# Performance work log

Measured on AMD Instinct MI355X. Metric: run time of the kernel, lower is better.

The kernel has to match this reference:

```python
import jax, jax.numpy as jnp
import numpy as np

PF = 8
BITS = 4
T, D, O, A = 1024, 2048, 4096, 4  # tokens, in_dim, per-slice out_dim, max_deltas


def _dequant(qw, qz, sc):
    """GPTQ-style 4-bit dequant, single quant group (g_idx all zero).
    qw: [O, D//PF] int32 (nibbles packed along input dim)
    qz: [O//PF, 1] int32 (zero nibbles packed along output dim)
    sc: [O, 1] float scales
    returns W: [O, D] float32
    """
    Od, Kp = qw.shape
    shifts = jnp.arange(PF, dtype=jnp.int32) * BITS
    q = ((qw[:, :, None] >> shifts) & 0xF).reshape(Od, Kp * PF).astype(jnp.float32)
    z = ((qz[:, 0][:, None] >> shifts) & 0xF).reshape(Od)[:, None].astype(jnp.float32)
    return sc.astype(jnp.float32) * (q - z)


def _delta_slice(x, indices, qw_s, qz_s, sc_s):
    # per-token adapter dispatch: tokens with indices==a use delta weight a
    out = jnp.zeros((x.shape[0], qw_s.shape[1]), dtype=jnp.float32)
    for a in range(qw_s.shape[0]):  # fixed small loop over adapters
        W = _dequant(qw_s[a], qz_s[a], sc_s[a])           # [O, D]
        xm = jnp.where((indices == a)[:, None], x, 0.0)    # gather-by-mask
        out = out + xm @ W.T                               # [T, O]
    return out


def setup_inputs() -> dict:
    key = jax.random.key(0)
    ks = jax.random.split(key, 10)
    MAXI = np.int32(2147483647)
    return {
        "x": jax.random.normal(ks[0], (T, D), dtype=jnp.float32),
        "base_weight": jax.random.normal(ks[1], (2 * O, D), dtype=jnp.float32) * 0.02,
        "base_bias": jax.random.normal(ks[2], (2 * O,), dtype=jnp.float32) * 0.02,
        "qweight_0": jax.random.randint(ks[3], (A, O, D // PF), 0, MAXI, dtype=jnp.int32),
        "qweight_1": jax.random.randint(ks[4], (A, O, D // PF), 0, MAXI, dtype=jnp.int32),
        "qzeros_0": jax.random.randint(ks[5], (A, O // PF, 1), 0, MAXI, dtype=jnp.int32),
        "qzeros_1": jax.random.randint(ks[6], (A, O // PF, 1), 0, MAXI, dtype=jnp.int32),
        "scales_0": jax.random.uniform(ks[7], (A, O, 1), dtype=jnp.float32) * 1e-3,
        "scales_1": jax.random.uniform(ks[8], (A, O, 1), dtype=jnp.float32) * 1e-3,
        "g_idx_0": jnp.zeros((D,), dtype=jnp.int32),
        "g_idx_1": jnp.zeros((D,), dtype=jnp.int32),
        "indices": jax.random.randint(ks[9], (T,), 0, A, dtype=jnp.int32),
    }


def reference(x, base_weight, base_bias, qweight_0, qweight_1, qzeros_0, qzeros_1,
              scales_0, scales_1, g_idx_0, g_idx_1, indices):
    # base ColumnParallelLinear GEMM (+bias, skip_bias_add=False)
    out = x @ base_weight.T + base_bias  # [T, 2*O]
    # apply_delta_packed_nslice onto the two equal output slices
    d0 = _delta_slice(x, indices, qweight_0, qzeros_0, scales_0)
    d1 = _delta_slice(x, indices, qweight_1, qzeros_1, scales_1)
    return out + jnp.concatenate([d0, d1], axis=1)
```

## Files before the change

kernel.cpp:

```cpp
#include <hip/hip_runtime.h>
#include <hip/hip_bf16.h>
#include <stdint.h>

#define T_TOK 1024
#define DIN   2048
#define NOUT  8192
#define OSL   4096
#define ROWS_PAD 1408
#define BM 128
#define BN 128
#define BK 32

typedef _Float16 f16x8 __attribute__((ext_vector_type(8)));
typedef _Float16 f16x2 __attribute__((ext_vector_type(2)));
typedef float    f32x4 __attribute__((ext_vector_type(4)));

__device__ __forceinline__ void gload16(const void* gp, void* lp) {
  __builtin_amdgcn_global_load_lds(
      (__attribute__((address_space(1))) void*)gp,
      (__attribute__((address_space(3))) void*)lp, 16, 0, 0);
}

__device__ __forceinline__ f16x2 u2h(uint32_t u) {
  union { uint32_t u; f16x2 h; } c; c.u = u; return c.h;
}

__device__ __forceinline__ f16x8 cvt_interleave(float4 f0, float4 f1) {
  f16x8 h;
  h[0] = (_Float16)f0.x; h[1] = (_Float16)f1.x;
  h[2] = (_Float16)f0.y; h[3] = (_Float16)f1.y;
  h[4] = (_Float16)f0.z; h[5] = (_Float16)f1.z;
  h[6] = (_Float16)f0.w; h[7] = (_Float16)f1.w;
  return h;
}

template<bool FULL>
__global__ void prep_all(const float* __restrict__ x, const float* __restrict__ wb,
                         const int* __restrict__ qw0, const int* __restrict__ qw1,
                         const int* __restrict__ qz0, const int* __restrict__ qz1,
                         const float* __restrict__ sc0, const float* __restrict__ sc1,
                         const int* __restrict__ indices,
                         _Float16* __restrict__ xh,
                         _Float16* __restrict__ wout,
                         int* __restrict__ inv, int* __restrict__ meta)
{
  const int b = blockIdx.x;
  const int tid = threadIdx.x;

  if (b == 0) {
    __shared__ int cnt[4], cur[4];
    if (tid < 4) cnt[tid] = 0;
    __syncthreads();
    for (int t = tid; t < T_TOK; t += 256) atomicAdd(&cnt[indices[t]], 1);
    __syncthreads();
    if (tid == 0) {
      int off = 0;
      for (int a = 0; a < 4; ++a) {
        meta[a] = off;
        meta[5 + a] = off + cnt[a];
        cur[a] = off;
        off = (off + cnt[a] + 127) & ~127;
      }
      meta[4] = off;
    }
    __syncthreads();
    for (int i = tid; i < ROWS_PAD; i += 256) inv[i] = -1;
    __syncthreads();
    for (int t = tid; t < T_TOK; t += 256) {
      int a = indices[t];
      int p = atomicAdd(&cur[a], 1);
      inv[p] = t;
    }
    return;
  }

  if (b <= 1 + T_TOK) {
    const int row = b - 1;
    const int d0 = tid * 8;
    f16x8 h;
    if (row < T_TOK) {
      const float* src = x + (size_t)row * DIN + d0;
      h = cvt_interleave(*(const float4*)src, *(const float4*)(src + 4));
    } else {
#pragma unroll
      for (int j = 0; j < 8; ++j) h[j] = (_Float16)0.0f;
    }
    *(f16x8*)(xh + (size_t)row * DIN + d0) = h;
    return;
  }

  const int n = b - (2 + T_TOK);
  const int d0 = tid * 8;
  const float* src = wb + (size_t)n * DIN + d0;
  union { f16x8 v; f16x2 p[4]; } wbr;
  wbr.v = cvt_interleave(*(const float4*)src, *(const float4*)(src + 4));

  if (!FULL) {
    *(f16x8*)(wout + (size_t)n * DIN + d0) = wbr.v;
    return;
  }

  const int sl = n >> 12;
  const int n_sl = n & (OSL - 1);
  const int* qw = sl ? qw1 : qw0;
  const int* qz = sl ? qz1 : qz0;
  const float* sc = sl ? sc1 : sc0;

#pragma unroll
  for (int a = 0; a < 4; ++a) {
    const uint32_t wv = (uint32_t)qw[((size_t)(a * OSL + n_sl)) * (DIN / 8) + tid];
    const int zw = qz[a * (OSL / 8) + (n_sl >> 3)];
    const float s = sc[(size_t)a * OSL + n_sl];
    const int z = (zw >> ((n_sl & 7) << 2)) & 0xF;
    f16x2 s2; s2[0] = s2[1] = (_Float16)s;
    f16x2 k2; k2[0] = k2[1] = (_Float16)(float)(-(1024 + z));
    union { f16x8 v; f16x2 p[4]; } h;
#pragma unroll
    for (int j = 0; j < 4; ++j) {
      uint32_t t0 = ((wv >> (4 * j)) & 0x000F000Fu) | 0x64006400u;
      h.p[j] = (u2h(t0) + k2) * s2 + wbr.p[j];
    }
    *(f16x8*)(wout + ((size_t)(a * NOUT) + n) * DIN + d0) = h.v;
  }
}

__global__ __launch_bounds__(256) void kslim(
    const _Float16* __restrict__ xh, const _Float16* __restrict__ weff,
    const float* __restrict__ bias,
    const int* __restrict__ inv, const int* __restrict__ meta,
    float* __restrict__ out)
{
  const int m0 = blockIdx.y * BM;
  if (m0 >= meta[4]) return;
  int ad = 0;
  if (m0 >= meta[1]) ad = 1;
  if (m0 >= meta[2]) ad = 2;
  if (m0 >= meta[3]) ad = 3;
  if (m0 >= meta[5 + ad]) return;

  const int n0 = blockIdx.x * BN;
  const int tid  = threadIdx.x;
  const int wave = tid >> 6;
  const int lane = tid & 63;
  const int quad = lane >> 4;
  const int l16  = lane & 15;
  const int wm = (wave & 1) << 6;
  const int wn = (wave >> 1) << 6;

  __shared__ __align__(16) char smem[16384];

  f32x4 acc[4][4];
#pragma unroll
  for (int i = 0; i < 4; ++i)
#pragma unroll
    for (int j = 0; j < 4; ++j) acc[i][j] = (f32x4)0.0f;

  const int kch = (((tid & 3) ^ ((tid >> 3) & 3)) << 3);
  const int rloc = tid >> 2;
  int r0 = inv[m0 + rloc];       if (r0 < 0) r0 = T_TOK;
  int r1 = inv[m0 + rloc + 64];  if (r1 < 0) r1 = T_TOK;
  const _Float16* ag0 = xh + (size_t)r0 * DIN + kch;
  const _Float16* ag1 = xh + (size_t)r1 * DIN + kch;
  const _Float16* bg0 = weff + ((size_t)(ad * NOUT) + n0 + rloc) * DIN + kch;
  const _Float16* bg1 = bg0 + (size_t)64 * DIN;
  char* sa0 = smem +         wave * 1024;
  char* sa1 = smem +  4096 + wave * 1024;
  char* sb0 = smem +  8192 + wave * 1024;
  char* sb1 = smem + 12288 + wave * 1024;

  const int qoff = ((quad ^ ((l16 >> 1) & 3)) << 4);

  for (int k0 = 0; k0 < DIN; k0 += BK) {
    gload16(ag0, sa0);
    gload16(ag1, sa1);
    gload16(bg0, sb0);
    gload16(bg1, sb1);
    __syncthreads();

    f16x8 af[4], bfr[4];
#pragma unroll
    for (int t = 0; t < 4; ++t)
      af[t] = *(const f16x8*)(smem + (wm + t * 16 + l16) * 64 + qoff);
#pragma unroll
    for (int t = 0; t < 4; ++t)
      bfr[t] = *(const f16x8*)(smem + 8192 + (wn + t * 16 + l16) * 64 + qoff);
#pragma unroll
    for (int mt = 0; mt < 4; ++mt)
#pragma unroll
      for (int nt = 0; nt < 4; ++nt)
        acc[mt][nt] = __builtin_amdgcn_mfma_f32_16x16x32_f16(af[mt], bfr[nt], acc[mt][nt], 0, 0, 0);
    __syncthreads();

    ag0 += BK; ag1 += BK; bg0 += BK; bg1 += BK;
  }

#pragma unroll
  for (int mt = 0; mt < 4; ++mt) {
    const int rowb = m0 + wm + mt * 16 + quad * 4;
    int tk[4];
#pragma unroll
    for (int r = 0; r < 4; ++r) tk[r] = inv[rowb + r];
#pragma unroll
    for (int nt = 0; nt < 4; ++nt) {
      const int col = n0 + wn + nt * 16 + l16;
      const float bv = bias[col];
#pragma unroll
      for (int r = 0; r < 4; ++r) {
        if (tk[r] >= 0)
          out[(size_t)tk[r] * NOUT + col] = acc[mt][nt][r] + bv;
      }
    }
  }
}

__global__ __launch_bounds__(256) void kdq(
    const _Float16* __restrict__ xh, const _Float16* __restrict__ wbh,
    const int* __restrict__ qw0, const int* __restrict__ qw1,
    const int* __restrict__ qz0, const int* __restrict__ qz1,
    const float* __restrict__ sc0, const float* __restrict__ sc1,
    const float* __restrict__ bias,
    const int* __restrict__ inv, const int* __restrict__ meta,
    float* __restrict__ out)
{
  const int m0 = blockIdx.y * BM;
  if (m0 >= meta[4]) return;
  int ad = 0;
  if (m0 >= meta[1]) ad = 1;
  if (m0 >= meta[2]) ad = 2;
  if (m0 >= meta[3]) ad = 3;
  if (m0 >= meta[5 + ad]) return;

  const int n0 = blockIdx.x * BN;
  const int sl = n0 >> 12;
  const int tid  = threadIdx.x;
  const int wave = tid >> 6;
  const int lane = tid & 63;
  const int quad = lane >> 4;
  const int l16  = lane & 15;
  const int wm = (wave & 1) << 6;
  const int wn = (wave >> 1) << 6;

  __shared__ __align__(16) char smem[16384];

  f32x4 acc[4][4];
#pragma unroll
  for (int i = 0; i < 4; ++i)
#pragma unroll
    for (int j = 0; j < 4; ++j) acc[i][j] = (f32x4)0.0f;

  const int kch = (((tid & 3) ^ ((tid >> 3) & 3)) << 3);
  const int rloc = tid >> 2;
  int r0 = inv[m0 + rloc];       if (r0 < 0) r0 = T_TOK;
  int r1 = inv[m0 + rloc + 64];  if (r1 < 0) r1 = T_TOK;
  const _Float16* ag0 = xh + (size_t)r0 * DIN + kch;
  const _Float16* ag1 = xh + (size_t)r1 * DIN + kch;
  char* sa0 = smem + wave * 1024;
  char* sa1 = smem + 4096 + wave * 1024;

  const int o_local = tid >> 1;
  const int o = n0 + o_local;
  const int o_sl = o & (OSL - 1);
  const int* qw = (sl ? qw1 : qw0) + ((size_t)ad * OSL + o_sl) * (DIN / 8) + ((tid & 1) << 1);
  const int zw = (sl ? qz1 : qz0)[ad * (OSL / 8) + (o_sl >> 3)];
  const float s = (sl ? sc1 : sc0)[(size_t)ad * OSL + o_sl];
  const int z = (zw >> ((o_sl & 7) << 2)) & 0xF;
  f16x2 s2; s2[0] = s2[1] = (_Float16)s;
  f16x2 k2; k2[0] = k2[1] = (_Float16)(float)(-(1024 + z));
  const _Float16* wbhp = wbh + (size_t)o * DIN + ((tid & 1) << 4);

  const int bswz = (o_local >> 1) & 3;
  char* bb = smem + 8192 + o_local * 64;
  char* bw0 = bb + (((((tid & 1) << 1)    ) ^ bswz) << 4);
  char* bw1 = bb + (((((tid & 1) << 1) | 1) ^ bswz) << 4);
  const int qoff = ((quad ^ ((l16 >> 1) & 3)) << 4);

  for (int k0 = 0; k0 < DIN; k0 += BK) {
    gload16(ag0, sa0);
    gload16(ag1, sa1);
    int2 wv = *(const int2*)qw;
    union { f16x8 v; f16x2 p[4]; } wA, wB;
    wA.v = *(const f16x8*)wbhp;
    wB.v = *(const f16x8*)(wbhp + 8);
    const uint32_t wx = (uint32_t)wv.x, wy = (uint32_t)wv.y;
    union { f16x8 v; f16x2 p[4]; } h0, h1;
#pragma unroll
    for (int j = 0; j < 4; ++j) {
      uint32_t t0 = ((wx >> (4 * j)) & 0x000F000Fu) | 0x64006400u;
      uint32_t t1 = ((wy >> (4 * j)) & 0x000F000Fu) | 0x64006400u;
      h0.p[j] = (u2h(t0) + k2) * s2 + wA.p[j];
      h1.p[j] = (u2h(t1) + k2) * s2 + wB.p[j];
    }
    *(f16x8*)bw0 = h0.v;
    *(f16x8*)bw1 = h1.v;
    __syncthreads();

    f16x8 af[4], bfr[4];
#pragma unroll
    for (int t = 0; t < 4; ++t)
      af[t] = *(const f16x8*)(smem + (wm + t * 16 + l16) * 64 + qoff);
#pragma unroll
    for (int t = 0; t < 4; ++t)
      bfr[t] = *(const f16x8*)(smem + 8192 + (wn + t * 16 + l16) * 64 + qoff);
#pragma unroll
    for (int mt = 0; mt < 4; ++mt)
#pragma unroll
      for (int nt = 0; nt < 4; ++nt)
        acc[mt][nt] = __builtin_amdgcn_mfma_f32_16x16x32_f16(af[mt], bfr[nt], acc[mt][nt], 0, 0, 0);
    __syncthreads();

    ag0 += BK; ag1 += BK; qw += 4; wbhp += BK;
  }

#pragma unroll
  for (int mt = 0; mt < 4; ++mt) {
    const int rowb = m0 + wm + mt * 16 + quad * 4;
    int tk[4];
#pragma unroll
    for (int r = 0; r < 4; ++r) tk[r] = inv[rowb + r];
#pragma unroll
    for (int nt = 0; nt < 4; ++nt) {
      const int col = n0 + wn + nt * 16 + l16;
      const float bv = bias[col];
#pragma unroll
      for (int r = 0; r < 4; ++r) {
        if (tk[r] >= 0)
          out[(size_t)tk[r] * NOUT + col] = acc[mt][nt][r] + bv;
      }
    }
  }
}

extern "C" void kernel_launch(void* const* d_in, const int* in_sizes, int n_in,
                              void* d_out, int out_size, void* d_ws, size_t ws_size,
                              hipStream_t stream) {
  const float* x    = (const float*)d_in[0];
  const float* wb   = (const float*)d_in[1];
  const float* bias = (const float*)d_in[2];
  const int*   qw0  = (const int*)d_in[3];
  const int*   qw1  = (const int*)d_in[4];
  const int*   qz0  = (const int*)d_in[5];
  const int*   qz1  = (const int*)d_in[6];
  const float* sc0  = (const float*)d_in[7];
  const float* sc1  = (const float*)d_in[8];
  const int*   indices = (const int*)d_in[11];
  float* out = (float*)d_out;

  char* w = (char*)d_ws;
  _Float16* xh = (_Float16*)w;
  size_t off = (size_t)(T_TOK + 1) * DIN * 2;
  int* inv  = (int*)(w + off);
  int* meta = inv + ROWS_PAD;
  size_t woff = (off + (size_t)ROWS_PAD * 4 + 64 + 255) & ~(size_t)255;
  _Float16* wout = (_Float16*)(w + woff);
  const bool full = ws_size >= woff + (size_t)4 * NOUT * DIN * 2;

  const int nprep = 2 + T_TOK + NOUT;
  dim3 g(NOUT / BN, ROWS_PAD / BM, 1);

  if (full) {
    prep_all<true><<<nprep, 256, 0, stream>>>(x, wb, qw0, qw1, qz0, qz1, sc0, sc1,
                                              indices, xh, wout, inv, meta);
    kslim<<<g, 256, 0, stream>>>(xh, wout, bias, inv, meta, out);
  } else {
    prep_all<false><<<nprep, 256, 0, stream>>>(x, wb, qw0, qw1, qz0, qz1, sc0, sc1,
                                               indices, xh, wout, inv, meta);
    kdq<<<g, 256, 0, stream>>>(xh, wout, qw0, qw1, qz0, qz1, sc0, sc1,
                               bias, inv, meta, out);
  }
}
```

Before: 227.7 us.

## Drop pre-dequantized weight path and software-pipeline fused dequant GEMM with double buffering

Removes the full-workspace path that materialized four dequantized fp16 effective weight matrices in the prep kernel. The fused dequant GEMM is now always used. It gets a double-buffered LDS pipeline with register prefetch of packed nibbles and base weights, explicit vmcnt/lgkmcnt waits, raw barriers and raised priority around the MFMAs. Block ids are remapped so neighbouring blocks share weight columns for better cache locality. This avoids writing and re-reading a large fp16 weight buffer, at the cost of redoing the dequant in every row tile and of more fragile hand scheduling.

```diff
diff --git a/kernel.cpp b/kernel.cpp
--- a/kernel.cpp
+++ b/kernel.cpp
@@ -1,5 +1,4 @@
 #include <hip/hip_runtime.h>
-#include <hip/hip_bf16.h>
 #include <stdint.h>
 
 #define T_TOK 1024
@@ -10,6 +9,8 @@
 #define BM 128
 #define BN 128
 #define BK 32
+#define NT (DIN / BK)
+#define BUF1 16384
 
 typedef _Float16 f16x8 __attribute__((ext_vector_type(8)));
 typedef _Float16 f16x2 __attribute__((ext_vector_type(2)));
@@ -34,15 +35,14 @@
   return h;
 }
 
-template<bool FULL>
-__global__ void prep_all(const float* __restrict__ x, const float* __restrict__ wb,
-                         const int* __restrict__ qw0, const int* __restrict__ qw1,
-                         const int* __restrict__ qz0, const int* __restrict__ qz1,
-                         const float* __restrict__ sc0, const float* __restrict__ sc1,
-                         const int* __restrict__ indices,
-                         _Float16* __restrict__ xh,
-                         _Float16* __restrict__ wout,
-                         int* __restrict__ inv, int* __restrict__ meta)
+#define VMCNT5() asm volatile("s_waitcnt vmcnt(5)" ::: "memory")
+#define VMCNT0() asm volatile("s_waitcnt vmcnt(0)" ::: "memory")
+#define LGKM0()  asm volatile("s_waitcnt lgkmcnt(0)" ::: "memory")
+
+__global__ void prep(const float* __restrict__ x, const float* __restrict__ wb,
+                     const int* __restrict__ indices,
+                     _Float16* __restrict__ xh, _Float16* __restrict__ wbh,
+                     int* __restrict__ inv, int* __restrict__ meta)
 {
   const int b = blockIdx.x;
   const int tid = threadIdx.x;
@@ -92,128 +92,11 @@
   const int n = b - (2 + T_TOK);
   const int d0 = tid * 8;
   const float* src = wb + (size_t)n * DIN + d0;
-  union { f16x8 v; f16x2 p[4]; } wbr;
-  wbr.v = cvt_interleave(*(const float4*)src, *(const float4*)(src + 4));
-
-  if (!FULL) {
-    *(f16x8*)(wout + (size_t)n * DIN + d0) = wbr.v;
-    return;
-  }
-
-  const int sl = n >> 12;
-  const int n_sl = n & (OSL - 1);
-  const int* qw = sl ? qw1 : qw0;
-  const int* qz = sl ? qz1 : qz0;
-  const float* sc = sl ? sc1 : sc0;
-
-#pragma unroll
-  for (int a = 0; a < 4; ++a) {
-    const uint32_t wv = (uint32_t)qw[((size_t)(a * OSL + n_sl)) * (DIN / 8) + tid];
-    const int zw = qz[a * (OSL / 8) + (n_sl >> 3)];
-    const float s = sc[(size_t)a * OSL + n_sl];
-    const int z = (zw >> ((n_sl & 7) << 2)) & 0xF;
-    f16x2 s2; s2[0] = s2[1] = (_Float16)s;
-    f16x2 k2; k2[0] = k2[1] = (_Float16)(float)(-(1024 + z));
-    union { f16x8 v; f16x2 p[4]; } h;
-#pragma unroll
-    for (int j = 0; j < 4; ++j) {
-      uint32_t t0 = ((wv >> (4 * j)) & 0x000F000Fu) | 0x64006400u;
-      h.p[j] = (u2h(t0) + k2) * s2 + wbr.p[j];
-    }
-    *(f16x8*)(wout + ((size_t)(a * NOUT) + n) * DIN + d0) = h.v;
-  }
-}
-
-__global__ __launch_bounds__(256) void kslim(
-    const _Float16* __restrict__ xh, const _Float16* __restrict__ weff,
-    const float* __restrict__ bias,
-    const int* __restrict__ inv, const int* __restrict__ meta,
-    float* __restrict__ out)
-{
-  const int m0 = blockIdx.y * BM;
-  if (m0 >= meta[4]) return;
-  int ad = 0;
-  if (m0 >= meta[1]) ad = 1;
-  if (m0 >= meta[2]) ad = 2;
-  if (m0 >= meta[3]) ad = 3;
-  if (m0 >= meta[5 + ad]) return;
-
-  const int n0 = blockIdx.x * BN;
-  const int tid  = threadIdx.x;
-  const int wave = tid >> 6;
-  const int lane = tid & 63;
-  const int quad = lane >> 4;
-  const int l16  = lane & 15;
-  const int wm = (wave & 1) << 6;
-  const int wn = (wave >> 1) << 6;
-
-  __shared__ __align__(16) char smem[16384];
-
-  f32x4 acc[4][4];
-#pragma unroll
-  for (int i = 0; i < 4; ++i)
-#pragma unroll
-    for (int j = 0; j < 4; ++j) acc[i][j] = (f32x4)0.0f;
-
-  const int kch = (((tid & 3) ^ ((tid >> 3) & 3)) << 3);
-  const int rloc = tid >> 2;
-  int r0 = inv[m0 + rloc];       if (r0 < 0) r0 = T_TOK;
-  int r1 = inv[m0 + rloc + 64];  if (r1 < 0) r1 = T_TOK;
-  const _Float16* ag0 = xh + (size_t)r0 * DIN + kch;
-  const _Float16* ag1 = xh + (size_t)r1 * DIN + kch;
-  const _Float16* bg0 = weff + ((size_t)(ad * NOUT) + n0 + rloc) * DIN + kch;
-  const _Float16* bg1 = bg0 + (size_t)64 * DIN;
-  char* sa0 = smem +         wave * 1024;
-  char* sa1 = smem +  4096 + wave * 1024;
-  char* sb0 = smem +  8192 + wave * 1024;
-  char* sb1 = smem + 12288 + wave * 1024;
-
-  const int qoff = ((quad ^ ((l16 >> 1) & 3)) << 4);
-
-  for (int k0 = 0; k0 < DIN; k0 += BK) {
-    gload16(ag0, sa0);
-    gload16(ag1, sa1);
-    gload16(bg0, sb0);
-    gload16(bg1, sb1);
-    __syncthreads();
-
-    f16x8 af[4], bfr[4];
-#pragma unroll
-    for (int t = 0; t < 4; ++t)
-      af[t] = *(const f16x8*)(smem + (wm + t * 16 + l16) * 64 + qoff);
-#pragma unroll
-    for (int t = 0; t < 4; ++t)
-      bfr[t] = *(const f16x8*)(smem + 8192 + (wn + t * 16 + l16) * 64 + qoff);
-#pragma unroll
-    for (int mt = 0; mt < 4; ++mt)
-#pragma unroll
-      for (int nt = 0; nt < 4; ++nt)
-        acc[mt][nt] = __builtin_amdgcn_mfma_f32_16x16x32_f16(af[mt], bfr[nt], acc[mt][nt], 0, 0, 0);
-    __syncthreads();
-
-    ag0 += BK; ag1 += BK; bg0 += BK; bg1 += BK;
-  }
-
-#pragma unroll
-  for (int mt = 0; mt < 4; ++mt) {
-    const int rowb = m0 + wm + mt * 16 + quad * 4;
-    int tk[4];
-#pragma unroll
-    for (int r = 0; r < 4; ++r) tk[r] = inv[rowb + r];
-#pragma unroll
-    for (int nt = 0; nt < 4; ++nt) {
-      const int col = n0 + wn + nt * 16 + l16;
-      const float bv = bias[col];
-#pragma unroll
-      for (int r = 0; r < 4; ++r) {
-        if (tk[r] >= 0)
-          out[(size_t)tk[r] * NOUT + col] = acc[mt][nt][r] + bv;
-      }
-    }
-  }
-}
-
-__global__ __launch_bounds__(256) void kdq(
+  f16x8 v = cvt_interleave(*(const float4*)src, *(const float4*)(src + 4));
+  *(f16x8*)(wbh + (size_t)n * DIN + d0) = v;
+}
+
+__global__ __launch_bounds__(256) void kfuse(
     const _Float16* __restrict__ xh, const _Float16* __restrict__ wbh,
     const int* __restrict__ qw0, const int* __restrict__ qw1,
     const int* __restrict__ qz0, const int* __restrict__ qz1,
@@ -222,7 +105,10 @@
     const int* __restrict__ inv, const int* __restrict__ meta,
     float* __restrict__ out)
 {
-  const int m0 = blockIdx.y * BM;
+  const int id = blockIdx.y * 64 + blockIdx.x;
+  const int m0 = (id >> 6) * BM;
+  const int n0 = (((id & 7) << 3) | ((id >> 3) & 7)) * BN;
+
   if (m0 >= meta[4]) return;
   int ad = 0;
   if (m0 >= meta[1]) ad = 1;
@@ -230,7 +116,6 @@
   if (m0 >= meta[3]) ad = 3;
   if (m0 >= meta[5 + ad]) return;
 
-  const int n0 = blockIdx.x * BN;
   const int sl = n0 >> 12;
   const int tid  = threadIdx.x;
   const int wave = tid >> 6;
@@ -240,7 +125,7 @@
   const int wm = (wave & 1) << 6;
   const int wn = (wave >> 1) << 6;
 
-  __shared__ __align__(16) char smem[16384];
+  __shared__ __align__(16) char smem[32768];
 
   f32x4 acc[4][4];
 #pragma unroll
@@ -254,62 +139,109 @@
   int r1 = inv[m0 + rloc + 64];  if (r1 < 0) r1 = T_TOK;
   const _Float16* ag0 = xh + (size_t)r0 * DIN + kch;
   const _Float16* ag1 = xh + (size_t)r1 * DIN + kch;
-  char* sa0 = smem + wave * 1024;
-  char* sa1 = smem + 4096 + wave * 1024;
+  const int saoff0 = wave * 1024;
+  const int saoff1 = 4096 + wave * 1024;
 
   const int o_local = tid >> 1;
   const int o = n0 + o_local;
   const int o_sl = o & (OSL - 1);
-  const int* qw = (sl ? qw1 : qw0) + ((size_t)ad * OSL + o_sl) * (DIN / 8) + ((tid & 1) << 1);
+  const int* qwp = (sl ? qw1 : qw0) + ((size_t)ad * OSL + o_sl) * (DIN / 8) + ((tid & 1) << 1);
   const int zw = (sl ? qz1 : qz0)[ad * (OSL / 8) + (o_sl >> 3)];
   const float s = (sl ? sc1 : sc0)[(size_t)ad * OSL + o_sl];
   const int z = (zw >> ((o_sl & 7) << 2)) & 0xF;
   f16x2 s2; s2[0] = s2[1] = (_Float16)s;
   f16x2 k2; k2[0] = k2[1] = (_Float16)(float)(-(1024 + z));
-  const _Float16* wbhp = wbh + (size_t)o * DIN + ((tid & 1) << 4);
+  const _Float16* wbp = wbh + (size_t)o * DIN + ((tid & 1) << 4);
 
   const int bswz = (o_local >> 1) & 3;
-  char* bb = smem + 8192 + o_local * 64;
-  char* bw0 = bb + (((((tid & 1) << 1)    ) ^ bswz) << 4);
-  char* bw1 = bb + (((((tid & 1) << 1) | 1) ^ bswz) << 4);
+  const int bwoff0 = 8192 + o_local * 64 + (((((tid & 1) << 1)    ) ^ bswz) << 4);
+  const int bwoff1 = 8192 + o_local * 64 + (((((tid & 1) << 1) | 1) ^ bswz) << 4);
   const int qoff = ((quad ^ ((l16 >> 1) & 3)) << 4);
 
-  for (int k0 = 0; k0 < DIN; k0 += BK) {
-    gload16(ag0, sa0);
-    gload16(ag1, sa1);
-    int2 wv = *(const int2*)qw;
-    union { f16x8 v; f16x2 p[4]; } wA, wB;
-    wA.v = *(const f16x8*)wbhp;
-    wB.v = *(const f16x8*)(wbhp + 8);
-    const uint32_t wx = (uint32_t)wv.x, wy = (uint32_t)wv.y;
-    union { f16x8 v; f16x2 p[4]; } h0, h1;
+  auto LOADREGS = [&](int t, int2 &qv, f16x8 &wa, f16x8 &wb2) {
+    qv  = *(const int2*)(qwp + t * 4);
+    wa  = *(const f16x8*)(wbp + t * BK);
+    wb2 = *(const f16x8*)(wbp + t * BK + 8);
+  };
+  auto GLOADS = [&](int bb, int t) {
+    gload16(ag0 + t * BK, smem + bb + saoff0);
+    gload16(ag1 + t * BK, smem + bb + saoff1);
+  };
+  auto DEQW = [&](int bb, int2 qv, f16x8 wa, f16x8 wb2) {
+    const uint32_t wx = (uint32_t)qv.x, wy = (uint32_t)qv.y;
+    union U { f16x8 v; f16x2 p[4]; } A_, B_, h0, h1;
+    A_.v = wa; B_.v = wb2;
 #pragma unroll
     for (int j = 0; j < 4; ++j) {
       uint32_t t0 = ((wx >> (4 * j)) & 0x000F000Fu) | 0x64006400u;
       uint32_t t1 = ((wy >> (4 * j)) & 0x000F000Fu) | 0x64006400u;
-      h0.p[j] = (u2h(t0) + k2) * s2 + wA.p[j];
-      h1.p[j] = (u2h(t1) + k2) * s2 + wB.p[j];
-    }
-    *(f16x8*)bw0 = h0.v;
-    *(f16x8*)bw1 = h1.v;
-    __syncthreads();
-
-    f16x8 af[4], bfr[4];
+      h0.p[j] = (u2h(t0) + k2) * s2 + A_.p[j];
+      h1.p[j] = (u2h(t1) + k2) * s2 + B_.p[j];
+    }
+    *(f16x8*)(smem + bb + bwoff0) = h0.v;
+    *(f16x8*)(smem + bb + bwoff1) = h1.v;
+  };
+  auto COMPUTE = [&](int bb) {
+    f16x8 af[4], bf[4];
 #pragma unroll
     for (int t = 0; t < 4; ++t)
-      af[t] = *(const f16x8*)(smem + (wm + t * 16 + l16) * 64 + qoff);
+      af[t] = *(const f16x8*)(smem + bb + (wm + t * 16 + l16) * 64 + qoff);
 #pragma unroll
     for (int t = 0; t < 4; ++t)
-      bfr[t] = *(const f16x8*)(smem + 8192 + (wn + t * 16 + l16) * 64 + qoff);
+      bf[t] = *(const f16x8*)(smem + bb + 8192 + (wn + t * 16 + l16) * 64 + qoff);
+    __builtin_amdgcn_s_setprio(1);
 #pragma unroll
     for (int mt = 0; mt < 4; ++mt)
 #pragma unroll
       for (int nt = 0; nt < 4; ++nt)
-        acc[mt][nt] = __builtin_amdgcn_mfma_f32_16x16x32_f16(af[mt], bfr[nt], acc[mt][nt], 0, 0, 0);
-    __syncthreads();
-
-    ag0 += BK; ag1 += BK; qw += 4; wbhp += BK;
-  }
+        acc[mt][nt] = __builtin_amdgcn_mfma_f32_16x16x32_f16(af[mt], bf[nt], acc[mt][nt], 0, 0, 0);
+    __builtin_amdgcn_s_setprio(0);
+  };
+
+  int2 qvA, qvB;
+  f16x8 waA, wbA2, waB, wbB2;
+
+  LOADREGS(0, qvA, waA, wbA2);
+  GLOADS(0, 0);
+  LOADREGS(1, qvB, waB, wbB2);
+  GLOADS(BUF1, 1);
+  VMCNT5();
+  __builtin_amdgcn_sched_barrier(0);
+  DEQW(0, qvA, waA, wbA2);
+  LGKM0();
+  __builtin_amdgcn_s_barrier();
+
+  for (int t = 0; t < NT - 2; t += 2) {
+    LOADREGS(t + 2, qvA, waA, wbA2);
+    COMPUTE(0);
+    __builtin_amdgcn_s_barrier();
+    __builtin_amdgcn_sched_barrier(0);
+    GLOADS(0, t + 2);
+    VMCNT5();
+    __builtin_amdgcn_sched_barrier(0);
+    DEQW(BUF1, qvB, waB, wbB2);
+    LGKM0();
+    __builtin_amdgcn_s_barrier();
+
+    LOADREGS(t + 3, qvB, waB, wbB2);
+    COMPUTE(BUF1);
+    __builtin_amdgcn_s_barrier();
+    __builtin_amdgcn_sched_barrier(0);
+    GLOADS(BUF1, t + 3);
+    VMCNT5();
+    __builtin_amdgcn_sched_barrier(0);
+    DEQW(0, qvA, waA, wbA2);
+    LGKM0();
+    __builtin_amdgcn_s_barrier();
+  }
+
+  COMPUTE(0);
+  VMCNT0();
+  __builtin_amdgcn_sched_barrier(0);
+  DEQW(BUF1, qvB, waB, wbB2);
+  LGKM0();
+  __builtin_amdgcn_s_barrier();
+  COMPUTE(BUF1);
 
 #pragma unroll
   for (int mt = 0; mt < 4; ++mt) {
@@ -351,20 +283,9 @@
   int* inv  = (int*)(w + off);
   int* meta = inv + ROWS_PAD;
   size_t woff = (off + (size_t)ROWS_PAD * 4 + 64 + 255) & ~(size_t)255;
-  _Float16* wout = (_Float16*)(w + woff);
-  const bool full = ws_size >= woff + (size_t)4 * NOUT * DIN * 2;
-
-  const int nprep = 2 + T_TOK + NOUT;
-  dim3 g(NOUT / BN, ROWS_PAD / BM, 1);
-
-  if (full) {
-    prep_all<true><<<nprep, 256, 0, stream>>>(x, wb, qw0, qw1, qz0, qz1, sc0, sc1,
-                                              indices, xh, wout, inv, meta);
-    kslim<<<g, 256, 0, stream>>>(xh, wout, bias, inv, meta, out);
-  } else {
-    prep_all<false><<<nprep, 256, 0, stream>>>(x, wb, qw0, qw1, qz0, qz1, sc0, sc1,
-                                               indices, xh, wout, inv, meta);
-    kdq<<<g, 256, 0, stream>>>(xh, wout, qw0, qw1, qz0, qz1, sc0, sc1,
-                               bias, inv, meta, out);
-  }
-}
+  _Float16* wbh = (_Float16*)(w + woff);
+
+  prep<<<2 + T_TOK + NOUT, 256, 0, stream>>>(x, wb, indices, xh, wbh, inv, meta);
+  kfuse<<<dim3(64, 11), 256, 0, stream>>>(xh, wbh, qw0, qw1, qz0, qz1, sc0, sc1,
+                                          bias, inv, meta, out);
+}
```

New measurement: 247.0 us. 1.08x slower.

## Double-buffer LDS tiles in grouped GEMM kernel to overlap loads with MFMA

Applied to the files above, without the earlier changes.

The first GEMM kernel now uses two LDS buffers (32 KB instead of 16 KB). It issues the global-to-LDS loads for tile k+1 while running MFMAs on tile k, and drops one barrier per iteration. The goal is to hide global memory latency that the single-buffer load, sync, compute, sync loop left exposed. Doubling LDS use may lower occupancy. The second kernel only swaps BK for a literal 32 and is otherwise unchanged.

```diff
diff --git a/kernel.cpp b/kernel.cpp
--- a/kernel.cpp
+++ b/kernel.cpp
@@ -10,6 +10,8 @@
 #define BM 128
 #define BN 128
 #define BK 32
+#define NT (DIN / BK)
+#define BUFS 16384
 
 typedef _Float16 f16x8 __attribute__((ext_vector_type(8)));
 typedef _Float16 f16x2 __attribute__((ext_vector_type(2)));
@@ -147,7 +149,7 @@
   const int wm = (wave & 1) << 6;
   const int wn = (wave >> 1) << 6;
 
-  __shared__ __align__(16) char smem[16384];
+  __shared__ __align__(16) char smem[32768];
 
   f32x4 acc[4][4];
 #pragma unroll
@@ -163,36 +165,55 @@
   const _Float16* ag1 = xh + (size_t)r1 * DIN + kch;
   const _Float16* bg0 = weff + ((size_t)(ad * NOUT) + n0 + rloc) * DIN + kch;
   const _Float16* bg1 = bg0 + (size_t)64 * DIN;
-  char* sa0 = smem +         wave * 1024;
-  char* sa1 = smem +  4096 + wave * 1024;
-  char* sb0 = smem +  8192 + wave * 1024;
-  char* sb1 = smem + 12288 + wave * 1024;
+  const int saoff0 =        wave * 1024;
+  const int saoff1 = 4096 + wave * 1024;
+  const int sboff0 = 8192 + wave * 1024;
+  const int sboff1 = 12288 + wave * 1024;
 
   const int qoff = ((quad ^ ((l16 >> 1) & 3)) << 4);
 
-  for (int k0 = 0; k0 < DIN; k0 += BK) {
-    gload16(ag0, sa0);
-    gload16(ag1, sa1);
-    gload16(bg0, sb0);
-    gload16(bg1, sb1);
-    __syncthreads();
-
-    f16x8 af[4], bfr[4];
-#pragma unroll
-    for (int t = 0; t < 4; ++t)
-      af[t] = *(const f16x8*)(smem + (wm + t * 16 + l16) * 64 + qoff);
-#pragma unroll
-    for (int t = 0; t < 4; ++t)
-      bfr[t] = *(const f16x8*)(smem + 8192 + (wn + t * 16 + l16) * 64 + qoff);
-#pragma unroll
-    for (int mt = 0; mt < 4; ++mt)
-#pragma unroll
-      for (int nt = 0; nt < 4; ++nt)
-        acc[mt][nt] = __builtin_amdgcn_mfma_f32_16x16x32_f16(af[mt], bfr[nt], acc[mt][nt], 0, 0, 0);
-    __syncthreads();
-
-    ag0 += BK; ag1 += BK; bg0 += BK; bg1 += BK;
-  }
+#define STAGE(t, base)                                         \
+  do {                                                         \
+    gload16(ag0 + (size_t)(t) * BK, smem + (base) + saoff0);   \
+    gload16(ag1 + (size_t)(t) * BK, smem + (base) + saoff1);   \
+    gload16(bg0 + (size_t)(t) * BK, smem + (base) + sboff0);   \
+    gload16(bg1 + (size_t)(t) * BK, smem + (base) + sboff1);   \
+  } while (0)
+
+#define MFMASTEP(base)                                                        \
+  do {                                                                        \
+    f16x8 af[4], bfr[4];                                                      \
+    _Pragma("unroll")                                                         \
+    for (int tt = 0; tt < 4; ++tt)                                            \
+      af[tt] = *(const f16x8*)(smem + (base) + (wm + tt * 16 + l16) * 64 + qoff); \
+    _Pragma("unroll")                                                         \
+    for (int tt = 0; tt < 4; ++tt)                                            \
+      bfr[tt] = *(const f16x8*)(smem + (base) + 8192 + (wn + tt * 16 + l16) * 64 + qoff); \
+    _Pragma("unroll")                                                         \
+    for (int mt = 0; mt < 4; ++mt)                                            \
+      _Pragma("unroll")                                                       \
+      for (int nt = 0; nt < 4; ++nt)                                          \
+        acc[mt][nt] = __builtin_amdgcn_mfma_f32_16x16x32_f16(af[mt], bfr[nt], acc[mt][nt], 0, 0, 0); \
+  } while (0)
+
+  STAGE(0, 0);
+  __syncthreads();
+
+  for (int t = 0; t < NT - 2; t += 2) {
+    STAGE(t + 1, BUFS);
+    MFMASTEP(0);
+    __syncthreads();
+    STAGE(t + 2, 0);
+    MFMASTEP(BUFS);
+    __syncthreads();
+  }
+  STAGE(NT - 1, BUFS);
+  MFMASTEP(0);
+  __syncthreads();
+  MFMASTEP(BUFS);
+
+#undef STAGE
+#undef MFMASTEP
 
 #pragma unroll
   for (int mt = 0; mt < 4; ++mt) {
@@ -274,7 +295,7 @@
   char* bw1 = bb + (((((tid & 1) << 1) | 1) ^ bswz) << 4);
   const int qoff = ((quad ^ ((l16 >> 1) & 3)) << 4);
 
-  for (int k0 = 0; k0 < DIN; k0 += BK) {
+  for (int k0 = 0; k0 < DIN; k0 += 32) {
     gload16(ag0, sa0);
     gload16(ag1, sa1);
     int2 wv = *(const int2*)qw;
@@ -308,7 +329,7 @@
         acc[mt][nt] = __builtin_amdgcn_mfma_f32_16x16x32_f16(af[mt], bfr[nt], acc[mt][nt], 0, 0, 0);
     __syncthreads();
 
-    ag0 += BK; ag1 += BK; qw += 4; wbhp += BK;
+    ag0 += 32; ag1 += 32; qw += 4; wbhp += 32;
   }
 
 #pragma unroll
```

Result: slower. 239.2 us (+5.0%).
